# Performance work log

Hardware: AMD Instinct MI355X
Metric: run time of the kernel (lower is better)

Reference implementation:

```python
import jax, jax.numpy as jnp
import numpy as np

N_NODES = 50000

def _gat_conv(x, src, dst, W, a_src, a_dst, bias, num_nodes, concat, neg_slope=0.2):
    # x: [N, Fin]; W: [Fin, H*C]; a_src/a_dst: [H, C]; src/dst: [E]
    H, C = a_src.shape
    h = (x @ W).reshape(-1, H, C)                      # [N, H, C]
    alpha_s = jnp.einsum('nhc,hc->nh', h, a_src)        # [N, H]
    alpha_d = jnp.einsum('nhc,hc->nh', h, a_dst)        # [N, H]
    e = alpha_s[src] + alpha_d[dst]                     # [E, H]
    e = jax.nn.leaky_relu(e, neg_slope)
    # segment softmax over destination nodes
    m = jax.ops.segment_max(e, dst, num_segments=num_nodes)   # [N, H]
    ex = jnp.exp(e - m[dst])                                   # [E, H]
    denom = jax.ops.segment_sum(ex, dst, num_segments=num_nodes)  # [N, H]
    alpha = ex / denom[dst]                                    # [E, H]
    msg = h[src] * alpha[:, :, None]                            # [E, H, C]
    out = jax.ops.segment_sum(msg, dst, num_segments=num_nodes)  # [N, H, C]
    if concat:
        out = out.reshape(-1, H * C)
    else:
        out = out.mean(axis=1)
    return out + bias

def _add_self_loops(edge_index, num_nodes):
    loop = jnp.arange(num_nodes, dtype=edge_index.dtype)
    src = jnp.concatenate([edge_index[0], loop])
    dst = jnp.concatenate([edge_index[1], loop])
    return src, dst

def setup_inputs() -> dict:
    key = jax.random.key(0)
    ks = jax.random.split(key, 12)
    N, E = N_NODES, 800000
    in_c, hid, out_c, H = 128, 32, 64, 4
    x = jax.random.normal(ks[0], (N, in_c), dtype=jnp.float32)
    edge_index = jax.random.randint(ks[1], (2, E), 0, N, dtype=jnp.int64)
    edge_weight = jax.random.uniform(ks[2], (E,), dtype=jnp.float32)
    s1 = 1.0 / np.sqrt(in_c)
    s2 = 1.0 / np.sqrt(hid * H)
    W1 = jax.random.normal(ks[3], (in_c, H * hid), dtype=jnp.float32) * s1
    a_src1 = jax.random.normal(ks[4], (H, hid), dtype=jnp.float32) * s1
    a_dst1 = jax.random.normal(ks[5], (H, hid), dtype=jnp.float32) * s1
    b1 = jnp.zeros((H * hid,), dtype=jnp.float32)
    W2 = jax.random.normal(ks[6], (H * hid, out_c), dtype=jnp.float32) * s2
    a_src2 = jax.random.normal(ks[7], (1, out_c), dtype=jnp.float32) * s2
    a_dst2 = jax.random.normal(ks[8], (1, out_c), dtype=jnp.float32) * s2
    b2 = jnp.zeros((out_c,), dtype=jnp.float32)
    return {"x": x, "edge_index": edge_index, "edge_weight": edge_weight,
            "W1": W1, "a_src1": a_src1, "a_dst1": a_dst1, "b1": b1,
            "W2": W2, "a_src2": a_src2, "a_dst2": a_dst2, "b2": b2}

def reference(x, edge_index, edge_weight, W1, a_src1, a_dst1, b1, W2, a_src2, a_dst2, b2):
    # PyG GATConv with edge_dim unset ignores edge_weight; self-loops added by default
    N = x.shape[0]
    src, dst = _add_self_loops(edge_index, N)
    h = _gat_conv(x, src, dst, W1, a_src1, a_dst1, b1, N, concat=True)
    h = jax.nn.relu(h)
    out = _gat_conv(h, src, dst, W2, a_src2, a_dst2, b2, N, concat=False)
    return out
```

## Files before the change

kernel.cpp:

```cpp
#include <hip/hip_runtime.h>
#include <hip/hip_fp16.h>
#include <math.h>


#define NEG_SLOPE 0.2f
#define NBLKA 256
#define MAXNB 512
#define LDH 136

typedef _Float16 f16x8 __attribute__((ext_vector_type(8)));
typedef float f32x4 __attribute__((ext_vector_type(4)));
typedef unsigned int u32x4 __attribute__((ext_vector_type(4)));

__device__ __forceinline__ float leaky(float v) { return v > 0.f ? v : NEG_SLOPE * v; }

__global__ __launch_bounds__(256) void histc_gemm1_k(const int* __restrict__ ei, int E, int ET,
                                                     int* __restrict__ blkpref, int NB,
                                                     const float* __restrict__ W1,
                                                     const float* __restrict__ W2,
                                                     _Float16* __restrict__ w2t,
                                                     const float* __restrict__ X,
                                                     const float* __restrict__ aw_s,
                                                     const float* __restrict__ aw_d,
                                                     __half* __restrict__ Hh,
// ... 25 lines not shown
    return;
  }
  _Float16* xs = (_Float16*)smemf;
  _Float16* wt = xs + 64 * LDH;
  int n0 = (blockIdx.x - NBLKA) * 64;
  for (int i = t; i < 4096; i += 256) {
    int k = i >> 5, n4 = (i & 31) * 4;
    float4 wv = *(const float4*)&W1[k * 128 + n4];
    wt[(n4 + 0) * LDH + k] = (_Float16)wv.x;
    wt[(n4 + 1) * LDH + k] = (_Float16)wv.y;
    wt[(n4 + 2) * LDH + k] = (_Float16)wv.z;
    wt[(n4 + 3) * LDH + k] = (_Float16)wv.w;
  }
  for (int i = t; i < 2048; i += 256) {
    int r = i >> 5, c4 = i & 31;
    int n = n0 + r;
    float4 xv = (n < N) ? *(const float4*)&X[(size_t)n * 128 + c4 * 4]
                        : make_float4(0.f, 0.f, 0.f, 0.f);
    __half2 h0 = __floats2half2_rn(xv.x, xv.y);
    __half2 h1 = __floats2half2_rn(xv.z, xv.w);
    uint2 u; u.x = *(unsigned*)&h0; u.y = *(unsigned*)&h1;
    *(uint2*)&xs[r * LDH + c4 * 4] = u;
  }
  __syncthreads();
  int wv = t >> 6, l = t & 63;
  int row16 = l & 15, kg = l >> 4;
  f32x4 acc[8];
  #pragma unroll
  for (int j = 0; j < 8; ++j) acc[j] = (f32x4){0.f, 0.f, 0.f, 0.f};
  #pragma unroll
  for (int kk = 0; kk < 4; ++kk) {
    int kbase = kk * 32 + kg * 8;
    f16x8 afr = *(f16x8*)&xs[(wv * 16 + row16) * LDH + kbase];
    #pragma unroll
    for (int j = 0; j < 8; ++j) {
      f16x8 bfr = *(f16x8*)&wt[(j * 16 + row16) * LDH + kbase];
      acc[j] = __builtin_amdgcn_mfma_f32_16x16x32_f16(afr, bfr, acc[j], 0, 0, 0);
    }
  }
  __syncthreads();
  #pragma unroll
  for (int j = 0; j < 8; ++j) {
    int col = j * 16 + row16;
    #pragma unroll
    for (int r = 0; r < 4; ++r) {
      int row = wv * 16 + kg * 4 + r;
      xs[row * LDH + col] = (_Float16)acc[j][r];
    }
  }
  __syncthreads();
  for (int i = t; i < 1024; i += 256) {
    int r = i >> 4, c8 = i & 15;
    int n = n0 + r;
    if (n < N) ((u32x4*)Hh)[(size_t)n * 16 + c8] = *(u32x4*)&xs[r * LDH + c8 * 8];
  }
  {
    int r = t >> 2, h = t & 3;
    int n = n0 + r;
    float ps = 0.f, pd = 0.f;
    #pragma unroll
    for (int q = 0; q < 4; ++q) {
      f16x8 hv = *(f16x8*)&xs[r * LDH + h * 32 + q * 8];
      float4 s0 = *(const float4*)&aw_s[h * 32 + q * 8];
      float4 s1 = *(const float4*)&aw_s[h * 32 + q * 8 + 4];
      float4 d0 = *(const float4*)&aw_d[h * 32 + q * 8];
      float4 d1 = *(const float4*)&aw_d[h * 32 + q * 8 + 4];
      ps += (float)hv[0] * s0.x + (float)hv[1] * s0.y + (float)hv[2] * s0.z + (float)hv[3] * s0.w
          + (float)hv[4] * s1.x + (float)hv[5] * s1.y + (float)hv[6] * s1.z + (float)hv[7] * s1.w;
      pd += (float)hv[0] * d0.x + (float)hv[1] * d0.y + (float)hv[2] * d0.z + (float)hv[3] * d0.w
          + (float)hv[4] * d1.x + (float)hv[5] * d1.y + (float)hv[6] * d1.z + (float)hv[7] * d1.w;
    }
    if (n < N) { as[n * 4 + h] = ps; ad[n * 4 + h] = pd; }
  }
}

__global__ __launch_bounds__(256) void scan_blk_k(int* __restrict__ blkpref,
                                                  int* __restrict__ bbase) {
  __shared__ int sm[NBLKA];
  int b = blockIdx.x, t = threadIdx.x;
  int v = blkpref[b * NBLKA + t];
  sm[t] = v;
  __syncthreads();
  #pragma unroll
  for (int off = 1; off < NBLKA; off <<= 1) {
    int x = (t >= off) ? sm[t - off] : 0;
    __syncthreads();
    sm[t] += x;
    __syncthreads();
  }
  blkpref[b * NBLKA + t] = sm[t] - v;
  if (t == NBLKA - 1) bbase[b] = sm[t];
}

__global__ __launch_bounds__(512) void scan_bkt_k(int* __restrict__ bbase,
                                                  int* __restrict__ lcnt,
                                                  int* __restrict__ rowptr,
                                                  int NB, int N, int ET) {
  __shared__ int sm[512];
  int t = threadIdx.x;
  int v = (t < NB) ? bbase[t] : 0;
  sm[t] = v;
  __syncthreads();
  #pragma unroll
  for (int off = 1; off < 512; off <<= 1) {
    int x = (t >= off) ? sm[t - off] : 0;
    __syncthreads();
    sm[t] += x;
// ... 40 lines not shown
  if (t < 128) ncnt[t] = 0;
  __syncthreads();
  for (int r = e0 + t; r < e1; r += 256)
    atomicAdd(&ncnt[pairs[r] >> 17], 1);
  __syncthreads();
  if (t < 128) spre[t] = ncnt[t];
  __syncthreads();
  #pragma unroll
  for (int off = 1; off < 128; off <<= 1) {
    int x = (t < 128 && t >= off) ? spre[t - off] : 0;
    __syncthreads();
    if (t < 128) spre[t] += x;
    __syncthreads();
  }
  if (t < nn) {
    int base = e0 + spre[t] - ncnt[t];
    rowptr[nb0 + t] = base;
    lcur[t] = base;
  }
  __syncthreads();
  for (int r = e0 + t; r < e1; r += 256) {
    int p = pairs[r];
    int pos = atomicAdd(&lcur[p >> 17], 1);
    srcs[pos] = p & 0x1FFFF;
  }
  int lane = t & 63, wv = t >> 6;
  bool valid = (t < nn);
  int deg = valid ? ncnt[t] : 0;
  bool isS = valid && (deg <= 16);
  bool isM = valid && (deg > 16) && (deg <= 32);
  bool isB = valid && (deg > 32);
  unsigned long long ms = __ballot(isS);
  unsigned long long mm = __ballot(isM);
  unsigned long long mbm = __ballot(isB);
  if (lane == 0 && wv < 2) {
    wcS[wv] = __popcll(ms); wcM[wv] = __popcll(mm); wcB[wv] = __popcll(mbm);
  }
  __syncthreads();
  if (t == 0) {
    bS = atomicAdd(&lcnt[0],  wcS[0] + wcS[1]);
    bM = atomicAdd(&lcnt[8],  wcM[0] + wcM[1]);
    bB = atomicAdd(&lcnt[16], wcB[0] + wcB[1]);
  }
  __syncthreads();
  unsigned long long below = (lane == 0) ? 0ull : (~0ull >> (64 - lane));
  int offS = bS + ((wv == 1) ? wcS[0] : 0);
  int offM = bM + ((wv == 1) ? wcM[0] : 0);
  int offB = bB + ((wv == 1) ? wcB[0] : 0);
  if (isS) small_list[offS + __popcll(ms & below)]  = nb0 + t;
  if (isM) med_list[offM + __popcll(mm & below)]    = nb0 + t;
  if (isB) big_list[offB + __popcll(mbm & below)]   = nb0 + t;
}

__global__ __launch_bounds__(256) void gemm2_k(const __half* __restrict__ X,
                                               const _Float16* __restrict__ WT,
                                               const float* __restrict__ aw_s,
                                               const float* __restrict__ aw_d,
                                               __half* __restrict__ Hh,
                                               float* __restrict__ as,
                                               float* __restrict__ ad, int N) {
  __shared__ _Float16 xs[64 * LDH];
  __shared__ _Float16 wt[64 * LDH];
  int t = threadIdx.x;
  int n0 = blockIdx.x * 64;
  for (int i = t; i < 1024; i += 256) {
    int r = i >> 4, c8 = i & 15;
    *(u32x4*)&wt[r * LDH + c8 * 8] = ((const u32x4*)WT)[i];
  }
  for (int i = t; i < 1024; i += 256) {
    int r = i >> 4, c8 = i & 15;
    int n = n0 + r;
    u32x4 v = (n < N) ? ((const u32x4*)X)[(size_t)n * 16 + c8] : (u32x4){0, 0, 0, 0};
    *(u32x4*)&xs[r * LDH + c8 * 8] = v;
  }
  __syncthreads();
  int wv = t >> 6, l = t & 63;
  int row16 = l & 15, kg = l >> 4;
  f32x4 acc[4];
  #pragma unroll
  for (int j = 0; j < 4; ++j) acc[j] = (f32x4){0.f, 0.f, 0.f, 0.f};
  #pragma unroll
  for (int kk = 0; kk < 4; ++kk) {
    int kbase = kk * 32 + kg * 8;
    f16x8 afr = *(f16x8*)&xs[(wv * 16 + row16) * LDH + kbase];
    #pragma unroll
    for (int j = 0; j < 4; ++j) {
      f16x8 bfr = *(f16x8*)&wt[(j * 16 + row16) * LDH + kbase];
      acc[j] = __builtin_amdgcn_mfma_f32_16x16x32_f16(afr, bfr, acc[j], 0, 0, 0);
    }
  }
  __syncthreads();
  #pragma unroll
  for (int j = 0; j < 4; ++j) {
    int col = j * 16 + row16;
    #pragma unroll
    for (int r = 0; r < 4; ++r) {
      int row = wv * 16 + kg * 4 + r;
      xs[row * LDH + col] = (_Float16)acc[j][r];
    }
  }
  __syncthreads();
  for (int i = t; i < 512; i += 256) {
    int r = i >> 3, c8 = i & 7;
    int n = n0 + r;
    if (n < N) ((u32x4*)Hh)[(size_t)n * 8 + c8] = *(u32x4*)&xs[r * LDH + c8 * 8];
  }
  {
    int r = t >> 2, q = t & 3;
    int n = n0 + r;
    float ps = 0.f, pd = 0.f;
    #pragma unroll
    for (int qq = 0; qq < 2; ++qq) {
      f16x8 hv = *(f16x8*)&xs[r * LDH + q * 16 + qq * 8];
      float4 s0 = *(const float4*)&aw_s[q * 16 + qq * 8];
      float4 s1 = *(const float4*)&aw_s[q * 16 + qq * 8 + 4];
      float4 d0 = *(const float4*)&aw_d[q * 16 + qq * 8];
      float4 d1 = *(const float4*)&aw_d[q * 16 + qq * 8 + 4];
      ps += (float)hv[0] * s0.x + (float)hv[1] * s0.y + (float)hv[2] * s0.z + (float)hv[3] * s0.w
          + (float)hv[4] * s1.x + (float)hv[5] * s1.y + (float)hv[6] * s1.z + (float)hv[7] * s1.w;
      pd += (float)hv[0] * d0.x + (float)hv[1] * d0.y + (float)hv[2] * d0.z + (float)hv[3] * d0.w
          + (float)hv[4] * d1.x + (float)hv[5] * d1.y + (float)hv[6] * d1.z + (float)hv[7] * d1.w;
    }
    ps += __shfl_xor(ps, 1); ps += __shfl_xor(ps, 2);
    pd += __shfl_xor(pd, 1); pd += __shfl_xor(pd, 2);
    if (q == 0 && n < N) { as[n] = ps; ad[n] = pd; }
  }
}

__device__ __forceinline__ void load8h(const __half* p, float* f) {
  uint4 hv = *(const uint4*)p;
  float2 f0 = __half22float2(*(const __half2*)&hv.x);
  float2 f1 = __half22float2(*(const __half2*)&hv.y);
  float2 f2 = __half22float2(*(const __half2*)&hv.z);
  float2 f3 = __half22float2(*(const __half2*)&hv.w);
  f[0] = f0.x; f[1] = f0.y; f[2] = f1.x; f[3] = f1.y;
  f[4] = f2.x; f[5] = f2.y; f[6] = f3.x; f[7] = f3.y;
}

__global__ __launch_bounds__(256) void agg1_k(const int* __restrict__ rowptr,
                                              const int* __restrict__ srcs,
                                              const float* __restrict__ as,
                                              const float* __restrict__ ad,
                                              const __half* __restrict__ Hm,
                                              const float* __restrict__ bias,
                                              __half* __restrict__ out,
                                              const int* __restrict__ small_list,
                                              const int* __restrict__ med_list,
                                              const int* __restrict__ big_list,
                                              const int* __restrict__ lcnt,
                                              int SB, int MB) {
  if (blockIdx.x < (unsigned)SB) {
    __shared__ float al_sm[16][17][4];
    __shared__ int   sr_sm[16][16];
    int g  = threadIdx.x >> 4;
    int gl = threadIdx.x & 15;
    int gidx = blockIdx.x * 16 + g;
    if (gidx >= lcnt[0]) return;
    int n = small_list[gidx];
    int r0 = rowptr[n];
    int deg = rowptr[n + 1] - r0;
    float4 adn = *(const float4*)&ad[n * 4];

    float e0 = -INFINITY, e1 = -INFINITY, e2 = -INFINITY, e3 = -INFINITY;
    int s = 0;
    if (gl < deg) {
      s = srcs[r0 + gl];
      float4 av = *(const float4*)&as[s * 4];
      e0 = leaky(av.x + adn.x); e1 = leaky(av.y + adn.y);
      e2 = leaky(av.z + adn.z); e3 = leaky(av.w + adn.w);
    }
    sr_sm[g][gl] = s;
    float m0 = e0, m1 = e1, m2 = e2, m3 = e3;
    #pragma unroll
    for (int off = 8; off > 0; off >>= 1) {
      m0 = fmaxf(m0, __shfl_xor(m0, off, 16)); m1 = fmaxf(m1, __shfl_xor(m1, off, 16));
      m2 = fmaxf(m2, __shfl_xor(m2, off, 16)); m3 = fmaxf(m3, __shfl_xor(m3, off, 16));
    }
    float sc0 = (gl < deg) ? __expf(e0 - m0) : 0.f;
    float sc1 = (gl < deg) ? __expf(e1 - m1) : 0.f;
    float sc2 = (gl < deg) ? __expf(e2 - m2) : 0.f;
    float sc3 = (gl < deg) ? __expf(e3 - m3) : 0.f;
    float s0 = sc0, s1 = sc1, s2 = sc2, s3 = sc3;
    #pragma unroll
    for (int off = 8; off > 0; off >>= 1) {
      s0 += __shfl_xor(s0, off, 16); s1 += __shfl_xor(s1, off, 16);
      s2 += __shfl_xor(s2, off, 16); s3 += __shfl_xor(s3, off, 16);
    }
    *(float4*)&al_sm[g][gl][0] =
        make_float4(sc0 / s0, sc1 / s1, sc2 / s2, sc3 / s3);

    int h = gl >> 2;
    int cbase = gl * 8;
    float a0 = 0.f, a1 = 0.f, a2 = 0.f, a3 = 0.f,
          a4 = 0.f, a5 = 0.f, a6 = 0.f, a7 = 0.f;
    for (int j = 0; j < deg; j += 4) {
      #pragma unroll
      for (int u = 0; u < 4; ++u) {
        int idx = j + u;
        bool vU = idx < deg;
        int jj = vU ? idx : 0;
        int   sU  = sr_sm[g][jj];
        float alU = vU ? al_sm[g][jj][h] : 0.f;
        float f[8];
        load8h(&Hm[(size_t)sU * 128 + cbase], f);
        a0 += f[0] * alU; a1 += f[1] * alU; a2 += f[2] * alU; a3 += f[3] * alU;
        a4 += f[4] * alU; a5 += f[5] * alU; a6 += f[6] * alU; a7 += f[7] * alU;
      }
    }
    float4 b0 = *(const float4*)&bias[cbase];
    float4 b1 = *(const float4*)&bias[cbase + 4];
    __half2* dst = (__half2*)&out[(size_t)n * 128 + cbase];
    dst[0] = __floats2half2_rn(fmaxf(a0 + b0.x, 0.f), fmaxf(a1 + b0.y, 0.f));
    dst[1] = __floats2half2_rn(fmaxf(a2 + b0.z, 0.f), fmaxf(a3 + b0.w, 0.f));
    dst[2] = __floats2half2_rn(fmaxf(a4 + b1.x, 0.f), fmaxf(a5 + b1.y, 0.f));
    dst[3] = __floats2half2_rn(fmaxf(a6 + b1.z, 0.f), fmaxf(a7 + b1.w, 0.f));
    return;
  }
  if (blockIdx.x < (unsigned)(SB + MB)) {
    __shared__ float al_sm[8][33][4];
    __shared__ int   sr_sm[8][32];
    int g   = threadIdx.x >> 5;
    int l32 = threadIdx.x & 31;
    int gidx = (blockIdx.x - SB) * 8 + g;
    if (gidx >= lcnt[8]) return;
    int n = med_list[gidx];
    int r0 = rowptr[n];
    int deg = rowptr[n + 1] - r0;
    float4 adn = *(const float4*)&ad[n * 4];

    float e0 = -INFINITY, e1 = -INFINITY, e2 = -INFINITY, e3 = -INFINITY;
    int s = 0;
    if (l32 < deg) {
      s = srcs[r0 + l32];
      float4 av = *(const float4*)&as[s * 4];
      e0 = leaky(av.x + adn.x); e1 = leaky(av.y + adn.y);
      e2 = leaky(av.z + adn.z); e3 = leaky(av.w + adn.w);
    }
    sr_sm[g][l32] = s;
    float m0 = e0, m1 = e1, m2 = e2, m3 = e3;
    #pragma unroll
    for (int off = 16; off > 0; off >>= 1) {
      m0 = fmaxf(m0, __shfl_xor(m0, off, 32)); m1 = fmaxf(m1, __shfl_xor(m1, off, 32));
      m2 = fmaxf(m2, __shfl_xor(m2, off, 32)); m3 = fmaxf(m3, __shfl_xor(m3, off, 32));
    }
    float sc0 = (l32 < deg) ? __expf(e0 - m0) : 0.f;
    float sc1 = (l32 < deg) ? __expf(e1 - m1) : 0.f;
    float sc2 = (l32 < deg) ? __expf(e2 - m2) : 0.f;
    float sc3 = (l32 < deg) ? __expf(e3 - m3) : 0.f;
    float s0 = sc0, s1 = sc1, s2 = sc2, s3 = sc3;
    #pragma unroll
    for (int off = 16; off > 0; off >>= 1) {
      s0 += __shfl_xor(s0, off, 32); s1 += __shfl_xor(s1, off, 32);
      s2 += __shfl_xor(s2, off, 32); s3 += __shfl_xor(s3, off, 32);
    }
    *(float4*)&al_sm[g][l32][0] =
        make_float4(sc0 / s0, sc1 / s1, sc2 / s2, sc3 / s3);

    int cl = l32 & 15, grp2 = l32 >> 4, h = cl >> 2;
    int cbase = cl * 8;
    float a0 = 0.f, a1 = 0.f, a2 = 0.f, a3 = 0.f,
          a4 = 0.f, a5 = 0.f, a6 = 0.f, a7 = 0.f;
    for (int base = 0; base < deg; base += 8) {
      #pragma unroll
      for (int u = 0; u < 4; ++u) {
        int idx = base + grp2 * 4 + u;
        bool vU = idx < deg;
        int jj = vU ? idx : 0;
        int   sU  = sr_sm[g][jj];
        float alU = vU ? al_sm[g][jj][h] : 0.f;
        float f[8];
        load8h(&Hm[(size_t)sU * 128 + cbase], f);
        a0 += f[0] * alU; a1 += f[1] * alU; a2 += f[2] * alU; a3 += f[3] * alU;
        a4 += f[4] * alU; a5 += f[5] * alU; a6 += f[6] * alU; a7 += f[7] * alU;
      }
    }
    a0 += __shfl_xor(a0, 16); a1 += __shfl_xor(a1, 16);
    a2 += __shfl_xor(a2, 16); a3 += __shfl_xor(a3, 16);
    a4 += __shfl_xor(a4, 16); a5 += __shfl_xor(a5, 16);
    a6 += __shfl_xor(a6, 16); a7 += __shfl_xor(a7, 16);
    if (grp2 == 0) {
      float4 b0 = *(const float4*)&bias[cbase];
      float4 b1 = *(const float4*)&bias[cbase + 4];
      __half2* dst = (__half2*)&out[(size_t)n * 128 + cbase];
      dst[0] = __floats2half2_rn(fmaxf(a0 + b0.x, 0.f), fmaxf(a1 + b0.y, 0.f));
      dst[1] = __floats2half2_rn(fmaxf(a2 + b0.z, 0.f), fmaxf(a3 + b0.w, 0.f));
      dst[2] = __floats2half2_rn(fmaxf(a4 + b1.x, 0.f), fmaxf(a5 + b1.y, 0.f));
      dst[3] = __floats2half2_rn(fmaxf(a6 + b1.z, 0.f), fmaxf(a7 + b1.w, 0.f));
    }
    return;
  }
  __shared__ float al_sm[4][64][4];
  __shared__ int   sr_sm[4][64];
  int wv = threadIdx.x >> 6, lane = threadIdx.x & 63;
  int widx = (blockIdx.x - SB - MB) * 4 + wv;
  if (widx >= lcnt[16]) return;
  int n = big_list[widx];
  int r0 = rowptr[n], r1 = rowptr[n + 1];
  int deg = r1 - r0;
  int grp = lane >> 4, gl = lane & 15, h = gl >> 2;
  int cbase = gl * 8;
  float4 adn = *(const float4*)&ad[n * 4];

  float a0 = 0.f, a1 = 0.f, a2 = 0.f, a3 = 0.f,
        a4 = 0.f, a5 = 0.f, a6 = 0.f, a7 = 0.f;

  if (deg <= 64) {
    float e0 = -INFINITY, e1 = -INFINITY, e2 = -INFINITY, e3 = -INFINITY;
    int s = 0;
    if (lane < deg) {
      s = srcs[r0 + lane];
      float4 av = *(const float4*)&as[s * 4];
      e0 = leaky(av.x + adn.x); e1 = leaky(av.y + adn.y);
      e2 = leaky(av.z + adn.z); e3 = leaky(av.w + adn.w);
    }
    sr_sm[wv][lane] = s;
    float m0 = e0, m1 = e1, m2 = e2, m3 = e3;
    #pragma unroll
    for (int off = 32; off > 0; off >>= 1) {
      m0 = fmaxf(m0, __shfl_xor(m0, off)); m1 = fmaxf(m1, __shfl_xor(m1, off));
      m2 = fmaxf(m2, __shfl_xor(m2, off)); m3 = fmaxf(m3, __shfl_xor(m3, off));
    }
    float sc0 = (lane < deg) ? __expf(e0 - m0) : 0.f;
    float sc1 = (lane < deg) ? __expf(e1 - m1) : 0.f;
    float sc2 = (lane < deg) ? __expf(e2 - m2) : 0.f;
    float sc3 = (lane < deg) ? __expf(e3 - m3) : 0.f;
    float s0 = sc0, s1 = sc1, s2 = sc2, s3 = sc3;
    #pragma unroll
    for (int off = 32; off > 0; off >>= 1) {
      s0 += __shfl_xor(s0, off); s1 += __shfl_xor(s1, off);
      s2 += __shfl_xor(s2, off); s3 += __shfl_xor(s3, off);
    }
    *(float4*)&al_sm[wv][lane][0] =
        make_float4(sc0 / s0, sc1 / s1, sc2 / s2, sc3 / s3);

    for (int base = 0; base < deg; base += 16) {
      #pragma unroll
      for (int u = 0; u < 4; ++u) {
        int idx = base + grp * 4 + u;
        bool vU = idx < deg;
        int jj = vU ? idx : 0;
        int   sU  = sr_sm[wv][jj];
        float alU = vU ? al_sm[wv][jj][h] : 0.f;
        float f[8];
        load8h(&Hm[(size_t)sU * 128 + cbase], f);
        a0 += f[0] * alU; a1 += f[1] * alU; a2 += f[2] * alU; a3 += f[3] * alU;
        a4 += f[4] * alU; a5 += f[5] * alU; a6 += f[6] * alU; a7 += f[7] * alU;
      }
    }
  } else {
    float m0 = -INFINITY, m1 = -INFINITY, m2 = -INFINITY, m3 = -INFINITY;
    for (int r = r0 + lane; r < r1; r += 64) {
      int s = srcs[r];
      float4 av = *(const float4*)&as[s * 4];
      m0 = fmaxf(m0, leaky(av.x + adn.x)); m1 = fmaxf(m1, leaky(av.y + adn.y));
      m2 = fmaxf(m2, leaky(av.z + adn.z)); m3 = fmaxf(m3, leaky(av.w + adn.w));
    }
    #pragma unroll
    for (int off = 32; off > 0; off >>= 1) {
      m0 = fmaxf(m0, __shfl_xor(m0, off)); m1 = fmaxf(m1, __shfl_xor(m1, off));
      m2 = fmaxf(m2, __shfl_xor(m2, off)); m3 = fmaxf(m3, __shfl_xor(m3, off));
    }
    float s0 = 0.f, s1 = 0.f, s2 = 0.f, s3 = 0.f;
    for (int r = r0 + lane; r < r1; r += 64) {
      int s = srcs[r];
      float4 av = *(const float4*)&as[s * 4];
      s0 += __expf(leaky(av.x + adn.x) - m0); s1 += __expf(leaky(av.y + adn.y) - m1);
      s2 += __expf(leaky(av.z + adn.z) - m2); s3 += __expf(leaky(av.w + adn.w) - m3);
    }
    #pragma unroll
    for (int off = 32; off > 0; off >>= 1) {
      s0 += __shfl_xor(s0, off); s1 += __shfl_xor(s1, off);
      s2 += __shfl_xor(s2, off); s3 += __shfl_xor(s3, off);
    }
    float mhh = (h == 0) ? m0 : (h == 1) ? m1 : (h == 2) ? m2 : m3;
    float inv = 1.f / ((h == 0) ? s0 : (h == 1) ? s1 : (h == 2) ? s2 : s3);
    float adh = (h == 0) ? adn.x : (h == 1) ? adn.y : (h == 2) ? adn.z : adn.w;
    for (int r = r0; r < r1; r += 8) {
      int rA = r + grp, rB = rA + 4;
      bool vA = rA < r1, vB = rB < r1;
      int sA = srcs[vA ? rA : r0];
      int sB = srcs[vB ? rB : r0];
      float avA = as[sA * 4 + h], avB = as[sB * 4 + h];
      float alA = vA ? (__expf(leaky(avA + adh) - mhh) * inv) : 0.f;
      float alB = vB ? (__expf(leaky(avB + adh) - mhh) * inv) : 0.f;
      float fA[8], fB[8];
      load8h(&Hm[(size_t)sA * 128 + cbase], fA);
      load8h(&Hm[(size_t)sB * 128 + cbase], fB);
      a0 += fA[0] * alA + fB[0] * alB; a1 += fA[1] * alA + fB[1] * alB;
      a2 += fA[2] * alA + fB[2] * alB; a3 += fA[3] * alA + fB[3] * alB;
      a4 += fA[4] * alA + fB[4] * alB; a5 += fA[5] * alA + fB[5] * alB;
      a6 += fA[6] * alA + fB[6] * alB; a7 += fA[7] * alA + fB[7] * alB;
    }
  }
  a0 += __shfl_xor(a0, 16); a0 += __shfl_xor(a0, 32);
  a1 += __shfl_xor(a1, 16); a1 += __shfl_xor(a1, 32);
  a2 += __shfl_xor(a2, 16); a2 += __shfl_xor(a2, 32);
  a3 += __shfl_xor(a3, 16); a3 += __shfl_xor(a3, 32);
  a4 += __shfl_xor(a4, 16); a4 += __shfl_xor(a4, 32);
  a5 += __shfl_xor(a5, 16); a5 += __shfl_xor(a5, 32);
  a6 += __shfl_xor(a6, 16); a6 += __shfl_xor(a6, 32);
  a7 += __shfl_xor(a7, 16); a7 += __shfl_xor(a7, 32);
  if (grp == 0) {
    float4 b0 = *(const float4*)&bias[cbase];
    float4 b1 = *(const float4*)&bias[cbase + 4];
    __half2* dst = (__half2*)&out[(size_t)n * 128 + cbase];
    dst[0] = __floats2half2_rn(fmaxf(a0 + b0.x, 0.f), fmaxf(a1 + b0.y, 0.f));
    dst[1] = __floats2half2_rn(fmaxf(a2 + b0.z, 0.f), fmaxf(a3 + b0.w, 0.f));
    dst[2] = __floats2half2_rn(fmaxf(a4 + b1.x, 0.f), fmaxf(a5 + b1.y, 0.f));
    dst[3] = __floats2half2_rn(fmaxf(a6 + b1.z, 0.f), fmaxf(a7 + b1.w, 0.f));
  }
}

__global__ __launch_bounds__(256) void agg2_k(const int* __restrict__ rowptr,
                                              const int* __restrict__ srcs,
                                              const float* __restrict__ as,
                                              const float* __restrict__ ad,
                                              const __half* __restrict__ Hm,
                                              const float* __restrict__ bias,
                                              float* __restrict__ out,
                                              const int* __restrict__ small_list,
                                              const int* __restrict__ med_list,
                                              const int* __restrict__ big_list,
                                              const int* __restrict__ lcnt,
                                              int SB, int MB) {
  if (blockIdx.x < (unsigned)SB) {
    __shared__ float al_sm[16][17];
    __shared__ int   sr_sm[16][16];
    int g  = threadIdx.x >> 4;
    int gl = threadIdx.x & 15;
    int gidx = blockIdx.x * 16 + g;
    if (gidx >= lcnt[0]) return;
    int n = small_list[gidx];
    int r0 = rowptr[n];
    int deg = rowptr[n + 1] - r0;
    float adn = ad[n];

    float e = -INFINITY;
    int s = 0;
    if (gl < deg) { s = srcs[r0 + gl]; e = leaky(as[s] + adn); }
    sr_sm[g][gl] = s;
    float m = e;
    #pragma unroll
    for (int off = 8; off > 0; off >>= 1) m = fmaxf(m, __shfl_xor(m, off, 16));
    float sc = (gl < deg) ? __expf(e - m) : 0.f;
    float ssum = sc;
    #pragma unroll
    for (int off = 8; off > 0; off >>= 1) ssum += __shfl_xor(ssum, off, 16);
    al_sm[g][gl] = sc / ssum;

    int cbase = gl * 4;
    float a0 = 0.f, a1 = 0.f, a2 = 0.f, a3 = 0.f;
    for (int j = 0; j < deg; j += 4) {
      #pragma unroll
      for (int u = 0; u < 4; ++u) {
        int idx = j + u;
        bool vU = idx < deg;
        int jj = vU ? idx : 0;
        int   sU  = sr_sm[g][jj];
        float alU = vU ? al_sm[g][jj] : 0.f;
        uint2 hv = *(const uint2*)&Hm[(size_t)sU * 64 + cbase];
        float2 f0 = __half22float2(*(const __half2*)&hv.x);
        float2 f1 = __half22float2(*(const __half2*)&hv.y);
// ... 127 lines not shown
      float2 fB1 = __half22float2(*(const __half2*)&hvB.y);
      a0 += fA0.x * alA + fB0.x * alB; a1 += fA0.y * alA + fB0.y * alB;
      a2 += fA1.x * alA + fB1.x * alB; a3 += fA1.y * alA + fB1.y * alB;
    }
  }
  a0 += __shfl_xor(a0, 16); a0 += __shfl_xor(a0, 32);
  a1 += __shfl_xor(a1, 16); a1 += __shfl_xor(a1, 32);
  a2 += __shfl_xor(a2, 16); a2 += __shfl_xor(a2, 32);
  a3 += __shfl_xor(a3, 16); a3 += __shfl_xor(a3, 32);
  if (grp == 0) {
    float4 bv = *(const float4*)&bias[cbase];
    float4 o;
    o.x = a0 + bv.x; o.y = a1 + bv.y; o.z = a2 + bv.z; o.w = a3 + bv.w;
    *(float4*)&out[(size_t)n * 64 + cbase] = o;
  }
}

extern "C" void kernel_launch(void* const* d_in, const int* in_sizes, int n_in,
                              void* d_out, int out_size, void* d_ws, size_t ws_size,
                              hipStream_t stream) {
  const float* x   = (const float*)d_in[0];
  const int*   ei  = (const int*)d_in[1];
  const float* W1  = (const float*)d_in[3];
  const float* aS1 = (const float*)d_in[4];
  const float* aD1 = (const float*)d_in[5];
  const float* b1  = (const float*)d_in[6];
  const float* W2  = (const float*)d_in[7];
  const float* aS2 = (const float*)d_in[8];
  const float* aD2 = (const float*)d_in[9];
  const float* b2  = (const float*)d_in[10];

  const int N  = in_sizes[0] / 128;
  const int E  = in_sizes[2];
  const int ET = E + N;
  const int NB = (N + 127) >> 7;

  float* ws    = (float*)d_ws;
  __half* h1h  = (__half*)ws;
  __half* o1h  = (__half*)(ws + (size_t)N * 64);
  float* as1   = ws + (size_t)N * 128;
  float* ad1   = as1  + (size_t)4 * N;
  float* as2   = ad1  + (size_t)4 * N;
  float* ad2   = as2  + (size_t)N;
  int*   lcnt    = (int*)(ad2 + (size_t)N);
  int*   rowptr  = lcnt + 32;
  int*   bbase   = rowptr + N + 1;
  int*   blkpref = bbase + NB + 1;
  int*   small_list = blkpref + NB * NBLKA;
  int*   med_list   = small_list + N;
  int*   big_list   = med_list + N;
  int*   srcs   = big_list + N;
  _Float16* w2t = (_Float16*)(srcs + ET);
  int*   pairs_sep = (int*)(w2t + 64 * 128);
  __half* h2h  = h1h;
  float* out  = (float*)d_out;

  const int gb = (N + 63) / 64;
  const int sb = (N + 15) / 16;
  const int mb = (N + 7) / 8;
  const int bb = (N + 3) / 4;

  histc_gemm1_k<<<NBLKA + gb, 256, 0, stream>>>(ei, E, ET, blkpref, NB, W1, W2, w2t,
                                                x, aS1, aD1, h1h, as1, ad1, N);
  scan_blk_k<<<NB, 256, 0, stream>>>(blkpref, bbase);
  scan_bkt_k<<<1, 512, 0, stream>>>(bbase, lcnt, rowptr, NB, N, ET);
  passA_k<<<NBLKA, 256, 0, stream>>>(ei, E, ET, bbase, blkpref, pairs_sep, NB);
  passB_k<<<NB, 256, 0, stream>>>(pairs_sep, bbase, rowptr, srcs,
                                  small_list, med_list, big_list, lcnt, N);

  agg1_k<<<sb + mb + bb, 256, 0, stream>>>(rowptr, srcs, as1, ad1, h1h, b1, o1h,
                                           small_list, med_list, big_list, lcnt, sb, mb);

  gemm2_k<<<gb, 256, 0, stream>>>(o1h, w2t, aS2, aD2, h2h, as2, ad2, N);
  agg2_k<<<sb + mb + bb, 256, 0, stream>>>(rowptr, srcs, as2, ad2, h2h, b2, out,
                                           small_list, med_list, big_list, lcnt, sb, mb);
}
```

Measured before the change: 213.9 us.

## Split layer-1 aggregation into alpha pass plus per-head gathers over head-major features

Layer-1 features and outputs now use a head-major layout: a [4][N][32] half table instead of [N][128]. The gemm1 epilogue writes this layout and gemm2 reads it. The fused agg1 kernel is replaced by two stages. alpha1_k computes the softmax weights per edge and head and stores them in a new global alpha buffer. Four gath1_k launches, one per head, then gather a 32-wide head slice with 8 lanes per node, so each launch touches a smaller table that may stay cache-resident. The cost is writing and re-reading 4×ET alpha floats, reading srcs four times, three extra launches, and narrower 8-byte gather loads.

```diff
diff --git a/kernel.cpp b/kernel.cpp
--- a/kernel.cpp
+++ b/kernel.cpp
@@ -101,7 +101,9 @@
   for (int i = t; i < 1024; i += 256) {
     int r = i >> 4, c8 = i & 15;
     int n = n0 + r;
-    if (n < N) ((u32x4*)Hh)[(size_t)n * 16 + c8] = *(u32x4*)&xs[r * LDH + c8 * 8];
+    if (n < N)
+      *(u32x4*)&Hh[((size_t)(c8 >> 2) * N + n) * 32 + (c8 & 3) * 8] =
+          *(u32x4*)&xs[r * LDH + c8 * 8];
   }
   {
     int r = t >> 2, h = t & 3;
@@ -248,6 +250,204 @@
   if (isB) big_list[offB + __popcll(mbm & below)]   = nb0 + t;
 }
 
+__global__ __launch_bounds__(256) void alpha1_k(const int* __restrict__ rowptr,
+                                                const int* __restrict__ srcs,
+                                                const float* __restrict__ as,
+                                                const float* __restrict__ ad,
+                                                float* __restrict__ alpha,
+                                                const int* __restrict__ small_list,
+                                                const int* __restrict__ med_list,
+                                                const int* __restrict__ big_list,
+                                                const int* __restrict__ lcnt,
+                                                int SB, int MB, int ET) {
+  if (blockIdx.x < (unsigned)SB) {
+    int g  = threadIdx.x >> 4;
+    int gl = threadIdx.x & 15;
+    int gidx = blockIdx.x * 16 + g;
+    if (gidx >= lcnt[0]) return;
+    int n = small_list[gidx];
+    int r0 = rowptr[n];
+    int deg = rowptr[n + 1] - r0;
+    float4 adn = *(const float4*)&ad[n * 4];
+    float e0 = -INFINITY, e1 = -INFINITY, e2 = -INFINITY, e3 = -INFINITY;
+    if (gl < deg) {
+      int s = srcs[r0 + gl];
+      float4 av = *(const float4*)&as[s * 4];
+      e0 = leaky(av.x + adn.x); e1 = leaky(av.y + adn.y);
+      e2 = leaky(av.z + adn.z); e3 = leaky(av.w + adn.w);
+    }
+    float m0 = e0, m1 = e1, m2 = e2, m3 = e3;
+    #pragma unroll
+    for (int off = 8; off > 0; off >>= 1) {
+      m0 = fmaxf(m0, __shfl_xor(m0, off, 16)); m1 = fmaxf(m1, __shfl_xor(m1, off, 16));
+      m2 = fmaxf(m2, __shfl_xor(m2, off, 16)); m3 = fmaxf(m3, __shfl_xor(m3, off, 16));
+    }
+    float sc0 = (gl < deg) ? __expf(e0 - m0) : 0.f;
+    float sc1 = (gl < deg) ? __expf(e1 - m1) : 0.f;
+    float sc2 = (gl < deg) ? __expf(e2 - m2) : 0.f;
+    float sc3 = (gl < deg) ? __expf(e3 - m3) : 0.f;
+    float s0 = sc0, s1 = sc1, s2 = sc2, s3 = sc3;
+    #pragma unroll
+    for (int off = 8; off > 0; off >>= 1) {
+      s0 += __shfl_xor(s0, off, 16); s1 += __shfl_xor(s1, off, 16);
+      s2 += __shfl_xor(s2, off, 16); s3 += __shfl_xor(s3, off, 16);
+    }
+    if (gl < deg) {
+      int r = r0 + gl;
+      alpha[0 * ET + r] = sc0 / s0; alpha[1 * ET + r] = sc1 / s1;
+      alpha[2 * ET + r] = sc2 / s2; alpha[3 * ET + r] = sc3 / s3;
+    }
+    return;
+  }
+  if (blockIdx.x < (unsigned)(SB + MB)) {
+    int g   = threadIdx.x >> 5;
+    int l32 = threadIdx.x & 31;
+    int gidx = (blockIdx.x - SB) * 8 + g;
+    if (gidx >= lcnt[8]) return;
+    int n = med_list[gidx];
+    int r0 = rowptr[n];
+    int deg = rowptr[n + 1] - r0;
+    float4 adn = *(const float4*)&ad[n * 4];
+    float e0 = -INFINITY, e1 = -INFINITY, e2 = -INFINITY, e3 = -INFINITY;
+    if (l32 < deg) {
+      int s = srcs[r0 + l32];
+      float4 av = *(const float4*)&as[s * 4];
+      e0 = leaky(av.x + adn.x); e1 = leaky(av.y + adn.y);
+      e2 = leaky(av.z + adn.z); e3 = leaky(av.w + adn.w);
+    }
+    float m0 = e0, m1 = e1, m2 = e2, m3 = e3;
+    #pragma unroll
+    for (int off = 16; off > 0; off >>= 1) {
+      m0 = fmaxf(m0, __shfl_xor(m0, off, 32)); m1 = fmaxf(m1, __shfl_xor(m1, off, 32));
+      m2 = fmaxf(m2, __shfl_xor(m2, off, 32)); m3 = fmaxf(m3, __shfl_xor(m3, off, 32));
+    }
+    float sc0 = (l32 < deg) ? __expf(e0 - m0) : 0.f;
+    float sc1 = (l32 < deg) ? __expf(e1 - m1) : 0.f;
+    float sc2 = (l32 < deg) ? __expf(e2 - m2) : 0.f;
+    float sc3 = (l32 < deg) ? __expf(e3 - m3) : 0.f;
+    float s0 = sc0, s1 = sc1, s2 = sc2, s3 = sc3;
+    #pragma unroll
+    for (int off = 16; off > 0; off >>= 1) {
+      s0 += __shfl_xor(s0, off, 32); s1 += __shfl_xor(s1, off, 32);
+      s2 += __shfl_xor(s2, off, 32); s3 += __shfl_xor(s3, off, 32);
+    }
+    if (l32 < deg) {
+      int r = r0 + l32;
+      alpha[0 * ET + r] = sc0 / s0; alpha[1 * ET + r] = sc1 / s1;
+      alpha[2 * ET + r] = sc2 / s2; alpha[3 * ET + r] = sc3 / s3;
+    }
+    return;
+  }
+  int wv = threadIdx.x >> 6, lane = threadIdx.x & 63;
+  int widx = (blockIdx.x - SB - MB) * 4 + wv;
+  if (widx >= lcnt[16]) return;
+  int n = big_list[widx];
+  int r0 = rowptr[n], r1 = rowptr[n + 1];
+  int deg = r1 - r0;
+  float4 adn = *(const float4*)&ad[n * 4];
+  if (deg <= 64) {
+    float e0 = -INFINITY, e1 = -INFINITY, e2 = -INFINITY, e3 = -INFINITY;
+    if (lane < deg) {
+      int s = srcs[r0 + lane];
+      float4 av = *(const float4*)&as[s * 4];
+      e0 = leaky(av.x + adn.x); e1 = leaky(av.y + adn.y);
+      e2 = leaky(av.z + adn.z); e3 = leaky(av.w + adn.w);
+    }
+    float m0 = e0, m1 = e1, m2 = e2, m3 = e3;
+    #pragma unroll
+    for (int off = 32; off > 0; off >>= 1) {
+      m0 = fmaxf(m0, __shfl_xor(m0, off)); m1 = fmaxf(m1, __shfl_xor(m1, off));
+      m2 = fmaxf(m2, __shfl_xor(m2, off)); m3 = fmaxf(m3, __shfl_xor(m3, off));
+    }
+    float sc0 = (lane < deg) ? __expf(e0 - m0) : 0.f;
+    float sc1 = (lane < deg) ? __expf(e1 - m1) : 0.f;
+    float sc2 = (lane < deg) ? __expf(e2 - m2) : 0.f;
+    float sc3 = (lane < deg) ? __expf(e3 - m3) : 0.f;
+    float s0 = sc0, s1 = sc1, s2 = sc2, s3 = sc3;
+    #pragma unroll
+    for (int off = 32; off > 0; off >>= 1) {
+      s0 += __shfl_xor(s0, off); s1 += __shfl_xor(s1, off);
+      s2 += __shfl_xor(s2, off); s3 += __shfl_xor(s3, off);
+    }
+    if (lane < deg) {
+      int r = r0 + lane;
+      alpha[0 * ET + r] = sc0 / s0; alpha[1 * ET + r] = sc1 / s1;
+      alpha[2 * ET + r] = sc2 / s2; alpha[3 * ET + r] = sc3 / s3;
+    }
+  } else {
+    float m0 = -INFINITY, m1 = -INFINITY, m2 = -INFINITY, m3 = -INFINITY;
+    for (int r = r0 + lane; r < r1; r += 64) {
+      int s = srcs[r];
+      float4 av = *(const float4*)&as[s * 4];
+      m0 = fmaxf(m0, leaky(av.x + adn.x)); m1 = fmaxf(m1, leaky(av.y + adn.y));
+      m2 = fmaxf(m2, leaky(av.z + adn.z)); m3 = fmaxf(m3, leaky(av.w + adn.w));
+    }
+    #pragma unroll
+    for (int off = 32; off > 0; off >>= 1) {
+      m0 = fmaxf(m0, __shfl_xor(m0, off)); m1 = fmaxf(m1, __shfl_xor(m1, off));
+      m2 = fmaxf(m2, __shfl_xor(m2, off)); m3 = fmaxf(m3, __shfl_xor(m3, off));
+    }
+    float s0 = 0.f, s1 = 0.f, s2 = 0.f, s3 = 0.f;
+    for (int r = r0 + lane; r < r1; r += 64) {
+      int s = srcs[r];
+      float4 av = *(const float4*)&as[s * 4];
+      s0 += __expf(leaky(av.x + adn.x) - m0); s1 += __expf(leaky(av.y + adn.y) - m1);
+      s2 += __expf(leaky(av.z + adn.z) - m2); s3 += __expf(leaky(av.w + adn.w) - m3);
+    }
+    #pragma unroll
+    for (int off = 32; off > 0; off >>= 1) {
+      s0 += __shfl_xor(s0, off); s1 += __shfl_xor(s1, off);
+      s2 += __shfl_xor(s2, off); s3 += __shfl_xor(s3, off);
+    }
+    float i0 = 1.f / s0, i1 = 1.f / s1, i2 = 1.f / s2, i3 = 1.f / s3;
+    for (int r = r0 + lane; r < r1; r += 64) {
+      int s = srcs[r];
+      float4 av = *(const float4*)&as[s * 4];
+      alpha[0 * ET + r] = __expf(leaky(av.x + adn.x) - m0) * i0;
+      alpha[1 * ET + r] = __expf(leaky(av.y + adn.y) - m1) * i1;
+      alpha[2 * ET + r] = __expf(leaky(av.z + adn.z) - m2) * i2;
+      alpha[3 * ET + r] = __expf(leaky(av.w + adn.w) - m3) * i3;
+    }
+  }
+}
+
+__global__ __launch_bounds__(256) void gath1_k(const int* __restrict__ rowptr,
+                                               const int* __restrict__ srcs,
+                                               const float* __restrict__ alpha,
+                                               const __half* __restrict__ Hh,
+                                               const float* __restrict__ bias,
+                                               __half* __restrict__ out,
+                                               int N, int ET, int hs) {
+  int g  = threadIdx.x >> 3;
+  int l8 = threadIdx.x & 7;
+  int n = blockIdx.x * 32 + g;
+  if (n >= N) return;
+  int r0 = rowptr[n], r1 = rowptr[n + 1];
+  const __half* tab = Hh + (size_t)hs * N * 32;
+  const float*  al  = alpha + (size_t)hs * ET;
+  int c4 = l8 * 4;
+  float a0 = 0.f, a1 = 0.f, a2 = 0.f, a3 = 0.f;
+  for (int r = r0; r < r1; r += 4) {
+    #pragma unroll
+    for (int u = 0; u < 4; ++u) {
+      int rr = r + u;
+      bool v = rr < r1;
+      int idx = v ? rr : r0;
+      int sU = srcs[idx];
+      float alU = v ? al[idx] : 0.f;
+      uint2 hv = *(const uint2*)&tab[(size_t)sU * 32 + c4];
+      float2 f0 = __half22float2(*(const __half2*)&hv.x);
+      float2 f1 = __half22float2(*(const __half2*)&hv.y);
+      a0 += f0.x * alU; a1 += f0.y * alU; a2 += f1.x * alU; a3 += f1.y * alU;
+    }
+  }
+  float4 bv = *(const float4*)&bias[hs * 32 + c4];
+  __half2 o0 = __floats2half2_rn(fmaxf(a0 + bv.x, 0.f), fmaxf(a1 + bv.y, 0.f));
+  __half2 o1 = __floats2half2_rn(fmaxf(a2 + bv.z, 0.f), fmaxf(a3 + bv.w, 0.f));
+  uint2 ov; ov.x = *(unsigned*)&o0; ov.y = *(unsigned*)&o1;
+  *(uint2*)&out[((size_t)hs * N + n) * 32 + c4] = ov;
+}
+
 __global__ __launch_bounds__(256) void gemm2_k(const __half* __restrict__ X,
                                                const _Float16* __restrict__ WT,
                                                const float* __restrict__ aw_s,
@@ -266,7 +466,9 @@
   for (int i = t; i < 1024; i += 256) {
     int r = i >> 4, c8 = i & 15;
     int n = n0 + r;
-    u32x4 v = (n < N) ? ((const u32x4*)X)[(size_t)n * 16 + c8] : (u32x4){0, 0, 0, 0};
+    u32x4 v = (n < N)
+        ? *(const u32x4*)&X[((size_t)(c8 >> 2) * N + n) * 32 + (c8 & 3) * 8]
+        : (u32x4){0, 0, 0, 0};
     *(u32x4*)&xs[r * LDH + c8 * 8] = v;
   }
   __syncthreads();
@@ -320,290 +522,6 @@
     ps += __shfl_xor(ps, 1); ps += __shfl_xor(ps, 2);
     pd += __shfl_xor(pd, 1); pd += __shfl_xor(pd, 2);
     if (q == 0 && n < N) { as[n] = ps; ad[n] = pd; }
-  }
-}
-
-__device__ __forceinline__ void load8h(const __half* p, float* f) {
-  uint4 hv = *(const uint4*)p;
-  float2 f0 = __half22float2(*(const __half2*)&hv.x);
-  float2 f1 = __half22float2(*(const __half2*)&hv.y);
-  float2 f2 = __half22float2(*(const __half2*)&hv.z);
-  float2 f3 = __half22float2(*(const __half2*)&hv.w);
-  f[0] = f0.x; f[1] = f0.y; f[2] = f1.x; f[3] = f1.y;
-  f[4] = f2.x; f[5] = f2.y; f[6] = f3.x; f[7] = f3.y;
-}
-
-__global__ __launch_bounds__(256) void agg1_k(const int* __restrict__ rowptr,
-                                              const int* __restrict__ srcs,
-                                              const float* __restrict__ as,
-                                              const float* __restrict__ ad,
-                                              const __half* __restrict__ Hm,
-                                              const float* __restrict__ bias,
-                                              __half* __restrict__ out,
-                                              const int* __restrict__ small_list,
-                                              const int* __restrict__ med_list,
-                                              const int* __restrict__ big_list,
-                                              const int* __restrict__ lcnt,
-                                              int SB, int MB) {
-  if (blockIdx.x < (unsigned)SB) {
-    __shared__ float al_sm[16][17][4];
-    __shared__ int   sr_sm[16][16];
-    int g  = threadIdx.x >> 4;
-    int gl = threadIdx.x & 15;
-    int gidx = blockIdx.x * 16 + g;
-    if (gidx >= lcnt[0]) return;
-    int n = small_list[gidx];
-    int r0 = rowptr[n];
-    int deg = rowptr[n + 1] - r0;
-    float4 adn = *(const float4*)&ad[n * 4];
-
-    float e0 = -INFINITY, e1 = -INFINITY, e2 = -INFINITY, e3 = -INFINITY;
-    int s = 0;
-    if (gl < deg) {
-      s = srcs[r0 + gl];
-      float4 av = *(const float4*)&as[s * 4];
-      e0 = leaky(av.x + adn.x); e1 = leaky(av.y + adn.y);
-      e2 = leaky(av.z + adn.z); e3 = leaky(av.w + adn.w);
-    }
-    sr_sm[g][gl] = s;
-    float m0 = e0, m1 = e1, m2 = e2, m3 = e3;
-    #pragma unroll
-    for (int off = 8; off > 0; off >>= 1) {
-      m0 = fmaxf(m0, __shfl_xor(m0, off, 16)); m1 = fmaxf(m1, __shfl_xor(m1, off, 16));
-      m2 = fmaxf(m2, __shfl_xor(m2, off, 16)); m3 = fmaxf(m3, __shfl_xor(m3, off, 16));
-    }
-    float sc0 = (gl < deg) ? __expf(e0 - m0) : 0.f;
-    float sc1 = (gl < deg) ? __expf(e1 - m1) : 0.f;
-    float sc2 = (gl < deg) ? __expf(e2 - m2) : 0.f;
-    float sc3 = (gl < deg) ? __expf(e3 - m3) : 0.f;
-    float s0 = sc0, s1 = sc1, s2 = sc2, s3 = sc3;
-    #pragma unroll
-    for (int off = 8; off > 0; off >>= 1) {
-      s0 += __shfl_xor(s0, off, 16); s1 += __shfl_xor(s1, off, 16);
-      s2 += __shfl_xor(s2, off, 16); s3 += __shfl_xor(s3, off, 16);
-    }
-    *(float4*)&al_sm[g][gl][0] =
-        make_float4(sc0 / s0, sc1 / s1, sc2 / s2, sc3 / s3);
-
-    int h = gl >> 2;
-    int cbase = gl * 8;
-    float a0 = 0.f, a1 = 0.f, a2 = 0.f, a3 = 0.f,
-          a4 = 0.f, a5 = 0.f, a6 = 0.f, a7 = 0.f;
-    for (int j = 0; j < deg; j += 4) {
-      #pragma unroll
-      for (int u = 0; u < 4; ++u) {
-        int idx = j + u;
-        bool vU = idx < deg;
-        int jj = vU ? idx : 0;
-        int   sU  = sr_sm[g][jj];
-        float alU = vU ? al_sm[g][jj][h] : 0.f;
-        float f[8];
-        load8h(&Hm[(size_t)sU * 128 + cbase], f);
-        a0 += f[0] * alU; a1 += f[1] * alU; a2 += f[2] * alU; a3 += f[3] * alU;
-        a4 += f[4] * alU; a5 += f[5] * alU; a6 += f[6] * alU; a7 += f[7] * alU;
-      }
-    }
-    float4 b0 = *(const float4*)&bias[cbase];
-    float4 b1 = *(const float4*)&bias[cbase + 4];
-    __half2* dst = (__half2*)&out[(size_t)n * 128 + cbase];
-    dst[0] = __floats2half2_rn(fmaxf(a0 + b0.x, 0.f), fmaxf(a1 + b0.y, 0.f));
-    dst[1] = __floats2half2_rn(fmaxf(a2 + b0.z, 0.f), fmaxf(a3 + b0.w, 0.f));
-    dst[2] = __floats2half2_rn(fmaxf(a4 + b1.x, 0.f), fmaxf(a5 + b1.y, 0.f));
-    dst[3] = __floats2half2_rn(fmaxf(a6 + b1.z, 0.f), fmaxf(a7 + b1.w, 0.f));
-    return;
-  }
-  if (blockIdx.x < (unsigned)(SB + MB)) {
-    __shared__ float al_sm[8][33][4];
-    __shared__ int   sr_sm[8][32];
-    int g   = threadIdx.x >> 5;
-    int l32 = threadIdx.x & 31;
-    int gidx = (blockIdx.x - SB) * 8 + g;
-    if (gidx >= lcnt[8]) return;
-    int n = med_list[gidx];
-    int r0 = rowptr[n];
-    int deg = rowptr[n + 1] - r0;
-    float4 adn = *(const float4*)&ad[n * 4];
-
-    float e0 = -INFINITY, e1 = -INFINITY, e2 = -INFINITY, e3 = -INFINITY;
-    int s = 0;
-    if (l32 < deg) {
-      s = srcs[r0 + l32];
-      float4 av = *(const float4*)&as[s * 4];
-      e0 = leaky(av.x + adn.x); e1 = leaky(av.y + adn.y);
-      e2 = leaky(av.z + adn.z); e3 = leaky(av.w + adn.w);
-    }
-    sr_sm[g][l32] = s;
-    float m0 = e0, m1 = e1, m2 = e2, m3 = e3;
-    #pragma unroll
-    for (int off = 16; off > 0; off >>= 1) {
-      m0 = fmaxf(m0, __shfl_xor(m0, off, 32)); m1 = fmaxf(m1, __shfl_xor(m1, off, 32));
-      m2 = fmaxf(m2, __shfl_xor(m2, off, 32)); m3 = fmaxf(m3, __shfl_xor(m3, off, 32));
-    }
-    float sc0 = (l32 < deg) ? __expf(e0 - m0) : 0.f;
-    float sc1 = (l32 < deg) ? __expf(e1 - m1) : 0.f;
-    float sc2 = (l32 < deg) ? __expf(e2 - m2) : 0.f;
-    float sc3 = (l32 < deg) ? __expf(e3 - m3) : 0.f;
-    float s0 = sc0, s1 = sc1, s2 = sc2, s3 = sc3;
-    #pragma unroll
-    for (int off = 16; off > 0; off >>= 1) {
-      s0 += __shfl_xor(s0, off, 32); s1 += __shfl_xor(s1, off, 32);
-      s2 += __shfl_xor(s2, off, 32); s3 += __shfl_xor(s3, off, 32);
-    }
-    *(float4*)&al_sm[g][l32][0] =
-        make_float4(sc0 / s0, sc1 / s1, sc2 / s2, sc3 / s3);
-
-    int cl = l32 & 15, grp2 = l32 >> 4, h = cl >> 2;
-    int cbase = cl * 8;
-    float a0 = 0.f, a1 = 0.f, a2 = 0.f, a3 = 0.f,
-          a4 = 0.f, a5 = 0.f, a6 = 0.f, a7 = 0.f;
-    for (int base = 0; base < deg; base += 8) {
-      #pragma unroll
-      for (int u = 0; u < 4; ++u) {
-        int idx = base + grp2 * 4 + u;
-        bool vU = idx < deg;
-        int jj = vU ? idx : 0;
-        int   sU  = sr_sm[g][jj];
-        float alU = vU ? al_sm[g][jj][h] : 0.f;
-        float f[8];
-        load8h(&Hm[(size_t)sU * 128 + cbase], f);
-        a0 += f[0] * alU; a1 += f[1] * alU; a2 += f[2] * alU; a3 += f[3] * alU;
-        a4 += f[4] * alU; a5 += f[5] * alU; a6 += f[6] * alU; a7 += f[7] * alU;
-      }
-    }
-    a0 += __shfl_xor(a0, 16); a1 += __shfl_xor(a1, 16);
-    a2 += __shfl_xor(a2, 16); a3 += __shfl_xor(a3, 16);
-    a4 += __shfl_xor(a4, 16); a5 += __shfl_xor(a5, 16);
-    a6 += __shfl_xor(a6, 16); a7 += __shfl_xor(a7, 16);
-    if (grp2 == 0) {
-      float4 b0 = *(const float4*)&bias[cbase];
-      float4 b1 = *(const float4*)&bias[cbase + 4];
-      __half2* dst = (__half2*)&out[(size_t)n * 128 + cbase];
-      dst[0] = __floats2half2_rn(fmaxf(a0 + b0.x, 0.f), fmaxf(a1 + b0.y, 0.f));
-      dst[1] = __floats2half2_rn(fmaxf(a2 + b0.z, 0.f), fmaxf(a3 + b0.w, 0.f));
-      dst[2] = __floats2half2_rn(fmaxf(a4 + b1.x, 0.f), fmaxf(a5 + b1.y, 0.f));
-      dst[3] = __floats2half2_rn(fmaxf(a6 + b1.z, 0.f), fmaxf(a7 + b1.w, 0.f));
-    }
-    return;
-  }
-  __shared__ float al_sm[4][64][4];
-  __shared__ int   sr_sm[4][64];
-  int wv = threadIdx.x >> 6, lane = threadIdx.x & 63;
-  int widx = (blockIdx.x - SB - MB) * 4 + wv;
-  if (widx >= lcnt[16]) return;
-  int n = big_list[widx];
-  int r0 = rowptr[n], r1 = rowptr[n + 1];
-  int deg = r1 - r0;
-  int grp = lane >> 4, gl = lane & 15, h = gl >> 2;
-  int cbase = gl * 8;
-  float4 adn = *(const float4*)&ad[n * 4];
-
-  float a0 = 0.f, a1 = 0.f, a2 = 0.f, a3 = 0.f,
-        a4 = 0.f, a5 = 0.f, a6 = 0.f, a7 = 0.f;
-
-  if (deg <= 64) {
-    float e0 = -INFINITY, e1 = -INFINITY, e2 = -INFINITY, e3 = -INFINITY;
-    int s = 0;
-    if (lane < deg) {
-      s = srcs[r0 + lane];
-      float4 av = *(const float4*)&as[s * 4];
-      e0 = leaky(av.x + adn.x); e1 = leaky(av.y + adn.y);
-      e2 = leaky(av.z + adn.z); e3 = leaky(av.w + adn.w);
-    }
-    sr_sm[wv][lane] = s;
-    float m0 = e0, m1 = e1, m2 = e2, m3 = e3;
-    #pragma unroll
-    for (int off = 32; off > 0; off >>= 1) {
-      m0 = fmaxf(m0, __shfl_xor(m0, off)); m1 = fmaxf(m1, __shfl_xor(m1, off));
-      m2 = fmaxf(m2, __shfl_xor(m2, off)); m3 = fmaxf(m3, __shfl_xor(m3, off));
-    }
-    float sc0 = (lane < deg) ? __expf(e0 - m0) : 0.f;
-    float sc1 = (lane < deg) ? __expf(e1 - m1) : 0.f;
-    float sc2 = (lane < deg) ? __expf(e2 - m2) : 0.f;
-    float sc3 = (lane < deg) ? __expf(e3 - m3) : 0.f;
-    float s0 = sc0, s1 = sc1, s2 = sc2, s3 = sc3;
-    #pragma unroll
-    for (int off = 32; off > 0; off >>= 1) {
-      s0 += __shfl_xor(s0, off); s1 += __shfl_xor(s1, off);
-      s2 += __shfl_xor(s2, off); s3 += __shfl_xor(s3, off);
-    }
-    *(float4*)&al_sm[wv][lane][0] =
-        make_float4(sc0 / s0, sc1 / s1, sc2 / s2, sc3 / s3);
-
-    for (int base = 0; base < deg; base += 16) {
-      #pragma unroll
-      for (int u = 0; u < 4; ++u) {
-        int idx = base + grp * 4 + u;
-        bool vU = idx < deg;
-        int jj = vU ? idx : 0;
-        int   sU  = sr_sm[wv][jj];
-        float alU = vU ? al_sm[wv][jj][h] : 0.f;
-        float f[8];
-        load8h(&Hm[(size_t)sU * 128 + cbase], f);
-        a0 += f[0] * alU; a1 += f[1] * alU; a2 += f[2] * alU; a3 += f[3] * alU;
-        a4 += f[4] * alU; a5 += f[5] * alU; a6 += f[6] * alU; a7 += f[7] * alU;
-      }
-    }
-  } else {
-    float m0 = -INFINITY, m1 = -INFINITY, m2 = -INFINITY, m3 = -INFINITY;
-    for (int r = r0 + lane; r < r1; r += 64) {
-      int s = srcs[r];
-      float4 av = *(const float4*)&as[s * 4];
-      m0 = fmaxf(m0, leaky(av.x + adn.x)); m1 = fmaxf(m1, leaky(av.y + adn.y));
-      m2 = fmaxf(m2, leaky(av.z + adn.z)); m3 = fmaxf(m3, leaky(av.w + adn.w));
-    }
-    #pragma unroll
-    for (int off = 32; off > 0; off >>= 1) {
-      m0 = fmaxf(m0, __shfl_xor(m0, off)); m1 = fmaxf(m1, __shfl_xor(m1, off));
-      m2 = fmaxf(m2, __shfl_xor(m2, off)); m3 = fmaxf(m3, __shfl_xor(m3, off));
-    }
-    float s0 = 0.f, s1 = 0.f, s2 = 0.f, s3 = 0.f;
-    for (int r = r0 + lane; r < r1; r += 64) {
-      int s = srcs[r];
-      float4 av = *(const float4*)&as[s * 4];
-      s0 += __expf(leaky(av.x + adn.x) - m0); s1 += __expf(leaky(av.y + adn.y) - m1);
-      s2 += __expf(leaky(av.z + adn.z) - m2); s3 += __expf(leaky(av.w + adn.w) - m3);
-    }
-    #pragma unroll
-    for (int off = 32; off > 0; off >>= 1) {
-      s0 += __shfl_xor(s0, off); s1 += __shfl_xor(s1, off);
-      s2 += __shfl_xor(s2, off); s3 += __shfl_xor(s3, off);
-    }
-    float mhh = (h == 0) ? m0 : (h == 1) ? m1 : (h == 2) ? m2 : m3;
-    float inv = 1.f / ((h == 0) ? s0 : (h == 1) ? s1 : (h == 2) ? s2 : s3);
-    float adh = (h == 0) ? adn.x : (h == 1) ? adn.y : (h == 2) ? adn.z : adn.w;
-    for (int r = r0; r < r1; r += 8) {
-      int rA = r + grp, rB = rA + 4;
-      bool vA = rA < r1, vB = rB < r1;
-      int sA = srcs[vA ? rA : r0];
-      int sB = srcs[vB ? rB : r0];
-      float avA = as[sA * 4 + h], avB = as[sB * 4 + h];
-      float alA = vA ? (__expf(leaky(avA + adh) - mhh) * inv) : 0.f;
-      float alB = vB ? (__expf(leaky(avB + adh) - mhh) * inv) : 0.f;
-      float fA[8], fB[8];
-      load8h(&Hm[(size_t)sA * 128 + cbase], fA);
-      load8h(&Hm[(size_t)sB * 128 + cbase], fB);
-      a0 += fA[0] * alA + fB[0] * alB; a1 += fA[1] * alA + fB[1] * alB;
-      a2 += fA[2] * alA + fB[2] * alB; a3 += fA[3] * alA + fB[3] * alB;
-      a4 += fA[4] * alA + fB[4] * alB; a5 += fA[5] * alA + fB[5] * alB;
-      a6 += fA[6] * alA + fB[6] * alB; a7 += fA[7] * alA + fB[7] * alB;
-    }
-  }
-  a0 += __shfl_xor(a0, 16); a0 += __shfl_xor(a0, 32);
-  a1 += __shfl_xor(a1, 16); a1 += __shfl_xor(a1, 32);
-  a2 += __shfl_xor(a2, 16); a2 += __shfl_xor(a2, 32);
-  a3 += __shfl_xor(a3, 16); a3 += __shfl_xor(a3, 32);
-  a4 += __shfl_xor(a4, 16); a4 += __shfl_xor(a4, 32);
-  a5 += __shfl_xor(a5, 16); a5 += __shfl_xor(a5, 32);
-  a6 += __shfl_xor(a6, 16); a6 += __shfl_xor(a6, 32);
-  a7 += __shfl_xor(a7, 16); a7 += __shfl_xor(a7, 32);
-  if (grp == 0) {
-    float4 b0 = *(const float4*)&bias[cbase];
-    float4 b1 = *(const float4*)&bias[cbase + 4];
-    __half2* dst = (__half2*)&out[(size_t)n * 128 + cbase];
-    dst[0] = __floats2half2_rn(fmaxf(a0 + b0.x, 0.f), fmaxf(a1 + b0.y, 0.f));
-    dst[1] = __floats2half2_rn(fmaxf(a2 + b0.z, 0.f), fmaxf(a3 + b0.w, 0.f));
-    dst[2] = __floats2half2_rn(fmaxf(a4 + b1.x, 0.f), fmaxf(a5 + b1.y, 0.f));
-    dst[3] = __floats2half2_rn(fmaxf(a6 + b1.z, 0.f), fmaxf(a7 + b1.w, 0.f));
   }
 }
 
@@ -837,6 +755,7 @@
   int*   srcs   = big_list + N;
   _Float16* w2t = (_Float16*)(srcs + ET);
   int*   pairs_sep = (int*)(w2t + 64 * 128);
+  float* alpha  = (float*)(pairs_sep + ET);
   __half* h2h  = h1h;
   float* out  = (float*)d_out;
 
@@ -844,6 +763,7 @@
   const int sb = (N + 15) / 16;
   const int mb = (N + 7) / 8;
   const int bb = (N + 3) / 4;
+  const int g32 = (N + 31) / 32;
 
   histc_gemm1_k<<<NBLKA + gb, 256, 0, stream>>>(ei, E, ET, blkpref, NB, W1, W2, w2t,
                                                 x, aS1, aD1, h1h, as1, ad1, N);
@@ -853,8 +773,11 @@
   passB_k<<<NB, 256, 0, stream>>>(pairs_sep, bbase, rowptr, srcs,
                                   small_list, med_list, big_list, lcnt, N);
 
-  agg1_k<<<sb + mb + bb, 256, 0, stream>>>(rowptr, srcs, as1, ad1, h1h, b1, o1h,
-                                           small_list, med_list, big_list, lcnt, sb, mb);
+  alpha1_k<<<sb + mb + bb, 256, 0, stream>>>(rowptr, srcs, as1, ad1, alpha,
+                                             small_list, med_list, big_list, lcnt,
+                                             sb, mb, ET);
+  for (int hs = 0; hs < 4; ++hs)
+    gath1_k<<<g32, 256, 0, stream>>>(rowptr, srcs, alpha, h1h, b1, o1h, N, ET, hs);
 
   gemm2_k<<<gb, 256, 0, stream>>>(o1h, w2t, aS2, aD2, h2h, as2, ad2, N);
   agg2_k<<<sb + mb + bb, 256, 0, stream>>>(rowptr, srcs, as2, ad2, h2h, b2, out,
```

New measurement: 260.6 us. 1.22x slower.
